# Performance work log

Hardware: AMD Instinct MI355X
Metric: run time of the kernel (lower is better)

The kernel has to match this reference:

```python
import jax, jax.numpy as jnp
from jax import lax
import numpy as np

B, T, S, Q = 256, 128, 16, 16
E, K = 128, 20
VOCAB = 50000 + K  # vocab_size + num_blocks (key slots appended)


def prelu(x, a):
    return jnp.where(x > 0, x, a * x)


def setup_inputs() -> dict:
    key = jax.random.key(0)
    ks = jax.random.split(key, 12)
    story = jax.random.randint(ks[0], (B, T, S), 0, 50000, dtype=jnp.int64 if jax.config.jax_enable_x64 else jnp.int32)
    query = jax.random.randint(ks[1], (B, Q), 0, 50000, dtype=jnp.int64 if jax.config.jax_enable_x64 else jnp.int32)
    embed_table = jax.random.normal(ks[2], (VOCAB, E), jnp.float32) * 0.1
    embed_table = embed_table.at[0].set(0.0)  # padding_idx=0
    story_mask = jnp.ones((S, E), jnp.float32)
    query_mask = jnp.ones((Q, E), jnp.float32)
    prelu_a = jnp.ones((E,), jnp.float32)
    U = jax.random.normal(ks[3], (E, E), jnp.float32) * 0.1
    V = jax.random.normal(ks[4], (E, E), jnp.float32) * 0.1
    W = jax.random.normal(ks[5], (E, E), jnp.float32) * 0.1
    bias = jax.random.normal(ks[6], (E,), jnp.float32) * 0.1
    H = jax.random.normal(ks[7], (E, E), jnp.float32) * 0.1
    R = jax.random.normal(ks[8], (VOCAB, E), jnp.float32) * 0.1
    return {"story": story, "query": query, "embed_table": embed_table,
            "story_mask": story_mask, "query_mask": query_mask, "prelu_a": prelu_a,
            "U": U, "V": V, "W": W, "bias": bias, "H": H, "R": R}


def reference(story, query, embed_table, story_mask, query_mask, prelu_a, U, V, W, bias, H, R):
    # encode story: (B,T,S,E) * (S,E) summed over S -> (B,T,E)
    s_enc = jnp.sum(embed_table[story] * story_mask, axis=2)
    # encode query: (B,Q,E) * (Q,E) summed over Q -> (B,E)
    q_enc = jnp.sum(embed_table[query] * query_mask, axis=1)

    keys = embed_table[VOCAB - K:]              # (K,E) block keys
    state0 = jnp.broadcast_to(keys[None], (B, K, E))
    key_V = keys @ V.T                           # (K,E), loop-invariant

    def step(state, x):                          # state (B,K,E), x (B,E)
        gate = jax.nn.sigmoid(jnp.einsum('be,bke->bk', x, state) + x @ keys.T)  # (B,K)
        cand = prelu(jnp.einsum('bke,fe->bkf', state, U) + bias
                     + (x @ W.T)[:, None, :] + key_V[None], prelu_a)
        ns = state + gate[..., None] * cand
        norm = jnp.linalg.norm(ns, axis=-1, keepdims=True) + 1e-8
        ns = jnp.where(ns > 0, ns, 1.0) / norm   # Threshold(0,1) then L2-normalize
        return ns, None

    state, _ = lax.scan(step, state0, jnp.swapaxes(s_enc, 0, 1))  # scan over T

    # output module
    att = jax.nn.softmax(jnp.einsum('bke,be->bk', state, q_enc), axis=-1)
    u = jnp.einsum('bk,bke->be', att, state)
    y = prelu(q_enc + u @ H.T, prelu_a) @ R.T    # (B,VOCAB)
    return y
```

## Files before the change

### kernel.cpp

```cpp
#include <hip/hip_runtime.h>
#include <hip/hip_bf16.h>
#include <stdint.h>

#define BB 256
#define TT 128
#define SS 16
#define QQ 16
#define EE 128
#define KK 20
#define VOCAB 50020
#define KB_ROWS 10
#define XK_STR 24

typedef __attribute__((ext_vector_type(8))) _Float16 h8v;
typedef __attribute__((ext_vector_type(2))) __fp16 fp2v;
typedef __attribute__((ext_vector_type(4))) unsigned short u4h;
typedef __attribute__((ext_vector_type(4))) float f4v;
#define MFMA16(a,b,c) __builtin_amdgcn_mfma_f32_16x16x32_f16(a,b,c,0,0,0)

static __device__ __forceinline__ unsigned pk2u(fp2v h){
  union { fp2v h; unsigned u; } c; c.h = h; return c.u;
}
static __device__ __forceinline__ float pk_lo(fp2v h){ return (float)h[0]; }
static __device__ __forceinline__ float pk_hi(fp2v h){ return (float)h[1]; }
static __device__ __forceinline__ unsigned short h1u(_Float16 h){
  union { _Float16 h; unsigned short u; } c; c.h = h; return c.u;
}
static __device__ __forceinline__ void split2_8(const float* v, h8v& h, h8v& l){
  #pragma unroll
  for (int j=0;j<8;++j){
    _Float16 hb = (_Float16)v[j];
    float hf = (float)hb;
    h[j] = hb;
    l[j] = (_Float16)(v[j]-hf);
  }
}
static __device__ __forceinline__ float dpp_add16(float x){
  int v;
  v = __builtin_amdgcn_update_dpp(0, __float_as_int(x), 0xB1, 0xF, 0xF, true);
  x += __int_as_float(v);
  v = __builtin_amdgcn_update_dpp(0, __float_as_int(x), 0x4E, 0xF, 0xF, true);
  x += __int_as_float(v);
  v = __builtin_amdgcn_update_dpp(0, __float_as_int(x), 0x124, 0xF, 0xF, true);
  x += __int_as_float(v);
  v = __builtin_amdgcn_update_dpp(0, __float_as_int(x), 0x128, 0xF, 0xF, true);
  x += __int_as_float(v);
  return x;
}
template<int IMM>
static __device__ __forceinline__ u4h tr_read(unsigned va){
  u4h d;
  asm volatile("ds_read_b64_tr_b16 %0, %1 offset:%c2" : "=v"(d) : "v"(va), "i"(IMM));
  return d;
}
static __device__ __forceinline__ h8v cat8h(u4h a, u4h b){
  union { u4h p[2]; h8v v; } u; u.p[0]=a; u.p[1]=b; return u.v;
}
#define LDA(P,K4) cat8h(tr_read<(P)*4096+(K4)*1024>(va), tr_read<(P)*4096+(K4)*1024+128>(va))

static const size_t OFF_SENC = 0;
static const size_t OFF_QENC = OFF_SENC + (size_t)BB*TT*EE;
static const size_t OFF_CKF  = OFF_QENC + (size_t)BB*EE;
static const size_t OFF_XW   = OFF_CKF  + (size_t)KK*EE;
static const size_t OFF_Z    = OFF_XW   + (size_t)BB*TT*EE;
static const size_t OFF_XK   = OFF_Z    + (size_t)BB*EE;
static const size_t OFF_ST   = OFF_XK   + (size_t)BB*TT*XK_STR;

__global__ __launch_bounds__(256) void k_small(
    const int* __restrict__ query, const float* __restrict__ emb,
    const float* __restrict__ qmask, const float* __restrict__ V,
    const float* __restrict__ bias, float* __restrict__ qenc,
    float* __restrict__ Ckf)
{
  int tid = threadIdx.x;
  int bid = blockIdx.x;
  if (bid < BB/8){
    int row = bid*8 + (tid>>5);
    int e4 = (tid&31)*4;
    float4 acc = make_float4(0.f,0.f,0.f,0.f);
    #pragma unroll
    for (int s=0; s<QQ; ++s) {
      int id = query[row*QQ + s];
      float4 ev = *(const float4*)(emb + (size_t)id*EE + e4);
      float4 mv = *(const float4*)(qmask + s*EE + e4);
      acc.x += ev.x*mv.x; acc.y += ev.y*mv.y; acc.z += ev.z*mv.z; acc.w += ev.w*mv.w;
    }
    *(float4*)(qenc + (size_t)row*EE + e4) = acc;
  } else {
    int k = bid - BB/8;
    if (tid < 128){
      int f = tid;
      const float* key = emb + (size_t)(VOCAB-KK+k)*EE;
      const float* vr  = V + (size_t)f*EE;
      float acc = bias[f];
      for (int e=0; e<EE; e+=4) {
        float4 kv = *(const float4*)(key + e);
        float4 vv = *(const float4*)(vr + e);
        acc += kv.x*vv.x + kv.y*vv.y + kv.z*vv.z + kv.w*vv.w;
      }
      Ckf[k*EE + f] = acc;
    }
  }
}

__global__ __launch_bounds__(256) void k_enc_xw(
    const int* __restrict__ tok, const float* __restrict__ emb,
    const float* __restrict__ smask, const float* __restrict__ W,
    float* __restrict__ senc, float* __restrict__ xw,
    float* __restrict__ xk)
{
  __shared__ float xs[64*EE];
  __shared__ float keys_s[KK*EE];
  int tid = threadIdx.x;
  int r0 = blockIdx.x*64;
  for (int i=0;i<8;++i){
    int row = i*8 + (tid>>5);
    int e4 = (tid&31)*4;
    float4 acc = make_float4(0.f,0.f,0.f,0.f);
    #pragma unroll
    for (int s=0; s<SS; ++s) {
      int id = tok[(size_t)(r0+row)*SS + s];
      float4 ev = *(const float4*)(emb + (size_t)id*EE + e4);
      float4 mv = *(const float4*)(smask + s*EE + e4);
      acc.x += ev.x*mv.x; acc.y += ev.y*mv.y; acc.z += ev.z*mv.z; acc.w += ev.w*mv.w;
    }
    *(float4*)(xs + row*EE + e4) = acc;
    *(float4*)(senc + (size_t)(r0+row)*EE + e4) = acc;
  }
  for (int idx=tid; idx<KK*EE; idx+=256)
    keys_s[idx] = emb[(size_t)(VOCAB-KK + (idx>>7))*EE + (idx&127)];
  __syncthreads();
  int f  = tid & 127;
  int rh = tid >> 7;
  float acc[32];
  #pragma unroll
  for (int i=0;i<32;++i) acc[i]=0.f;
  const float* wr = W + (size_t)f*EE;
  for (int e4=0; e4<EE; e4+=4) {
    float4 w4 = *(const float4*)(wr + e4);
    #pragma unroll
    for (int rr=0; rr<32; ++rr) {
      float4 x4 = *(const float4*)(xs + (rh*32+rr)*EE + e4);
      acc[rr] += w4.x*x4.x + w4.y*x4.y + w4.z*x4.z + w4.w*x4.w;
    }
  }
  #pragma unroll
  for (int rr=0; rr<32; ++rr)
    xw[(size_t)(r0 + rh*32 + rr)*EE + f] = acc[rr];
  for (int i=0;i<5;++i){
    int task = tid + i*256;
    int r = task/KK, k = task - r*KK;
    float a = 0.f;
    for (int e=0; e<EE; e+=4){
      float4 x4 = *(const float4*)(xs + r*EE + e);
      float4 k4 = *(const float4*)(keys_s + k*EE + e);
      a += x4.x*k4.x + x4.y*k4.y + x4.z*k4.z + x4.w*k4.w;
    }
    int ki = k < 10 ? k : k + 2;
    xk[(size_t)(r0+r)*XK_STR + ki] = a;
  }
}

struct ScanLds {
  unsigned short st[2][2][EE][16];
  unsigned short xp[2][2][EE];
  float npart[2][4][16];
};

__global__ __launch_bounds__(256) void k_scan(
    const float* __restrict__ emb, const float* __restrict__ U,
    const float* __restrict__ senc, const float* __restrict__ xw,
    const float* __restrict__ xk, const float* __restrict__ Ckf,
    const float* __restrict__ prelu_a, float* __restrict__ zst)
{
  __shared__ ScanLds L;
  int tid = threadIdx.x;
  int bid = blockIdx.x;
  int b   = bid >> 1, kb = bid & 1;
  int l   = tid & 63, cg = tid >> 6;
  int q   = l >> 4,  c  = l & 15;
  int col[2] = { cg*32 + c, cg*32 + 16 + c };

  for (int idx = tid; idx < 2*2*EE*16; idx += 256) ((unsigned short*)L.st)[idx] = 0;
  __syncthreads();
  for (int idx = tid; idx < KB_ROWS*EE; idx += 256){
    int row = idx >> 7, e = idx & 127;
    float v = emb[(size_t)(VOCAB - KK + kb*KB_ROWS + row)*EE + e];
    _Float16 hb = (_Float16)v;
    _Float16 lb = (_Float16)(v - (float)hb);
    L.st[0][0][e][row] = h1u(hb);
    L.st[0][1][e][row] = h1u(lb);
  }
  h8v bh[2][4], bl[2][4];
  #pragma unroll
  for (int nt=0;nt<2;++nt)
    #pragma unroll
    for (int kk=0;kk<4;++kk){
      float tmp[8];
      const float* up = U + (size_t)col[nt]*EE + kk*32 + q*8;
      *(float4*)&tmp[0] = *(const float4*)up;
      *(float4*)&tmp[4] = *(const float4*)(up+4);
      split2_8(tmp, bh[nt][kk], bl[nt][kk]);
    }
  float Creg[2][4], pa2[2], nsv[2][4];
  bool realr[4];
  #pragma unroll
  for (int r=0;r<4;++r) realr[r] = (4*q + r) < KB_ROWS;
  #pragma unroll
  for (int nt=0;nt<2;++nt){
    pa2[nt] = prelu_a[col[nt]];
    #pragma unroll
    for (int r=0;r<4;++r){
      int lr = 4*q + r;
      Creg[nt][r] = realr[r] ? Ckf[(kb*KB_ROWS+lr)*EE + col[nt]] : 0.f;
      nsv[nt][r]  = realr[r] ? emb[(size_t)(VOCAB-KK+kb*KB_ROWS+lr)*EE + col[nt]] : 0.f;
    }
  }

  const float* xrow  = senc + (size_t)b*TT*EE;
  const float* xwrow = xw   + (size_t)b*TT*EE;
  const float* xkrow = xk   + (size_t)b*TT*XK_STR + kb*12;

  if (tid < EE){
    float v = xrow[tid];
    _Float16 hb = (_Float16)v;
    _Float16 lb = (_Float16)(v - (float)hb);
    L.xp[0][0][tid] = h1u(hb); L.xp[0][1][tid] = h1u(lb);
  }
  float xwc[2] = { xwrow[col[0]], xwrow[col[1]] };
  float xkc[4];
  {
    f4v xk4 = {0.f,0.f,0.f,0.f};
    if (q < 3) xk4 = *(const f4v*)(xkrow + 4*q);
    #pragma unroll
    for (int r=0;r<4;++r) xkc[r] = realr[r] ? xk4[r] : 0.f;
  }

  unsigned va0 = (unsigned)(uintptr_t)&L.st[0][0][0][0] + q*256 + c*8;
  __syncthreads();

  for (int t=0; t<TT; ++t){
    int p = t & 1, pn = p ^ 1;
    unsigned va = va0 + p*8192;
    const unsigned short (*xpp)[EE] = L.xp[p];

    float invr[4];
    if (t > 0){
      f4v p0 = *(const f4v*)&L.npart[p][0][4*q];
      f4v p1 = *(const f4v*)&L.npart[p][1][4*q];
      f4v p2 = *(const f4v*)&L.npart[p][2][4*q];
      f4v p3 = *(const f4v*)&L.npart[p][3][4*q];
      f4v ss = p0 + p1 + p2 + p3;
      #pragma unroll
      for (int r=0;r<4;++r)
        invr[r] = __builtin_amdgcn_rcpf(__builtin_amdgcn_sqrtf(ss[r]) + 1e-8f);
    } else {
      #pragma unroll
      for (int r=0;r<4;++r) invr[r] = 1.0f;
    }

    float nxv = 0.f, xwn[2] = {0.f,0.f};
    f4v xk4n = {0.f,0.f,0.f,0.f};
    if (t+1 < TT){
      if (tid < EE) nxv = xrow[(size_t)(t+1)*EE + tid];
      xwn[0] = xwrow[(size_t)(t+1)*EE + col[0]];
      xwn[1] = xwrow[(size_t)(t+1)*EE + col[1]];
      if (q < 3) xk4n = *(const f4v*)(xkrow + (size_t)(t+1)*XK_STR + 4*q);
    }

    h8v Ah[4] = { LDA(0,0), LDA(0,1), LDA(0,2), LDA(0,3) };
    h8v Al[4] = { LDA(1,0), LDA(1,1), LDA(1,2), LDA(1,3) };
    asm volatile("s_waitcnt lgkmcnt(0)" ::: "memory");
    __builtin_amdgcn_sched_barrier(0);

    f4v z4 = {0.f,0.f,0.f,0.f};
    f4v acc[2][2] = {{z4,z4},{z4,z4}};
    f4v gac[2] = {z4,z4};
    #pragma unroll
    for (int kk=0; kk<4; ++kk){
      int h = kk>>1;
      h8v xh = *(const h8v*)&xpp[0][kk*32 + q*8];
      h8v xl = *(const h8v*)&xpp[1][kk*32 + q*8];
      #pragma unroll
      for (int nt=0;nt<2;++nt){
        acc[nt][h] = MFMA16(Al[kk], bh[nt][kk], acc[nt][h]);
        acc[nt][h] = MFMA16(Ah[kk], bl[nt][kk], acc[nt][h]);
        acc[nt][h] = MFMA16(Ah[kk], bh[nt][kk], acc[nt][h]);
      }
      gac[h] = MFMA16(Al[kk], xh, gac[h]);
      gac[h] = MFMA16(Ah[kk], xl, gac[h]);
      gac[h] = MFMA16(Ah[kk], xh, gac[h]);
    }
    f4v acc0 = acc[0][0] + acc[0][1];
    f4v acc1 = acc[1][0] + acc[1][1];
    f4v gacc = gac[0] + gac[1];

    float s2[4];
    #pragma unroll
    for (int r=0;r<4;++r){
      float graw = gacc[r]*invr[r] + xkc[r];
      float g = __builtin_amdgcn_rcpf(1.0f + __builtin_amdgcn_exp2f(-1.442695040889f * graw));
      float s2r = 0.f;
      #pragma unroll
      for (int nt=0;nt<2;++nt){
        float so = nsv[nt][r] * invr[r];
        float cv = (nt ? acc1[r] : acc0[r])*invr[r] + Creg[nt][r] + xwc[nt];
        cv = cv > 0.f ? cv : pa2[nt]*cv;
        float n = so + g*cv;
        nsv[nt][r] = realr[r] ? (n > 0.f ? n : 1.0f) : 0.f;
        s2r += n*n;
      }
      s2[r] = dpp_add16(s2r);
    }
    if (c == 0){
      f4v np; np[0]=s2[0]; np[1]=s2[1]; np[2]=s2[2]; np[3]=s2[3];
      *(f4v*)&L.npart[pn][cg][4*q] = np;
    }

    #pragma unroll
    for (int nt=0;nt<2;++nt){
      float v0=nsv[nt][0], v1=nsv[nt][1], v2=nsv[nt][2], v3=nsv[nt][3];
      fp2v pa = __builtin_amdgcn_cvt_pkrtz(v0, v1);
      fp2v pb = __builtin_amdgcn_cvt_pkrtz(v2, v3);
      float r0 = v0 - pk_lo(pa);
      float r1 = v1 - pk_hi(pa);
      float r2 = v2 - pk_lo(pb);
      float r3 = v3 - pk_hi(pb);
      fp2v pc = __builtin_amdgcn_cvt_pkrtz(r0, r1);
      fp2v pd = __builtin_amdgcn_cvt_pkrtz(r2, r3);
      *(uint2*)&L.st[pn][0][col[nt]][4*q] = make_uint2(pk2u(pa), pk2u(pb));
      *(uint2*)&L.st[pn][1][col[nt]][4*q] = make_uint2(pk2u(pc), pk2u(pd));
    }
    if (t+1 < TT && tid < EE){
      _Float16 hb = (_Float16)nxv;
      _Float16 lb = (_Float16)(nxv - (float)hb);
      L.xp[pn][0][tid] = h1u(hb); L.xp[pn][1][tid] = h1u(lb);
    }
    xwc[0]=xwn[0]; xwc[1]=xwn[1];
    #pragma unroll
    for (int r=0;r<4;++r) xkc[r] = realr[r] ? xk4n[r] : 0.f;
    __syncthreads();
  }

  {
    int pf = TT & 1;
    f4v p0 = *(const f4v*)&L.npart[pf][0][4*q];
    f4v p1 = *(const f4v*)&L.npart[pf][1][4*q];
    f4v p2 = *(const f4v*)&L.npart[pf][2][4*q];
    f4v p3 = *(const f4v*)&L.npart[pf][3][4*q];
    f4v ss = p0 + p1 + p2 + p3;
    #pragma unroll
    for (int r=0;r<4;++r){
      if (realr[r]){
        float inv = __builtin_amdgcn_rcpf(__builtin_amdgcn_sqrtf(ss[r]) + 1e-8f);
        #pragma unroll
        for (int nt=0;nt<2;++nt)
          zst[((size_t)b*KK + kb*KB_ROWS + 4*q + r)*EE + col[nt]] = nsv[nt][r]*inv;
      }
    }
  }
}

__global__ __launch_bounds__(128) void k_tail(
    const float* __restrict__ zst, const float* __restrict__ qenc,
    const float* __restrict__ prelu_a, const float* __restrict__ H,
    float* __restrict__ zout)
{
  __shared__ float st[KK*EE];
  __shared__ float us[EE];
  __shared__ float red[2][KK];
  __shared__ float gs[KK];
  int b = blockIdx.x, tid = threadIdx.x;
  for (int i = tid; i < KK*EE; i += 128) st[i] = zst[(size_t)b*KK*EE + i];
  float qv = qenc[(size_t)b*EE + tid];
  __syncthreads();
  int wv = tid >> 6, ln = tid & 63;
  for (int k=0;k<KK;++k){
    float p = qv * st[k*EE + tid];
    #pragma unroll
    for (int off=32; off; off>>=1) p += __shfl_xor(p, off);
    if (ln == 0) red[wv][k] = p;
  }
  __syncthreads();
  if (tid == 0){
    float mx = -1e30f, gg[KK];
    for (int k=0;k<KK;++k){ float v = red[0][k]+red[1][k]; gg[k]=v; mx = fmaxf(mx, v); }
    float s = 0.f;
    for (int k=0;k<KK;++k){ float e_ = expf(gg[k]-mx); gg[k]=e_; s += e_; }
    for (int k=0;k<KK;++k) gs[k] = gg[k]/s;
  }
  __syncthreads();
  float u_ = 0.f;
  #pragma unroll
  for (int k=0;k<KK;++k) u_ += gs[k]*st[k*EE + tid];
  us[tid] = u_;
  __syncthreads();
  float hp = 0.f;
  const float* hr = H + (size_t)tid*EE;
  for (int e=0; e<EE; e+=4){
    float4 h4 = *(const float4*)(hr + e);
    float4 u4 = *(const float4*)(us + e);
    hp += h4.x*u4.x + h4.y*u4.y + h4.z*u4.z + h4.w*u4.w;
  }
  float zv = qv + hp;
  float pat = prelu_a[tid];
  zv = zv > 0.f ? zv : pat*zv;
  zout[(size_t)b*EE + tid] = zv;
}

__global__ __launch_bounds__(256) void k_out(
    const float* __restrict__ z, const float* __restrict__ R,
    float* __restrict__ y)
{
  int tid = threadIdx.x;
  int w = tid >> 6, l = tid & 63;
  int q = l >> 4, cc = l & 15;
  int b0 = blockIdx.y * 64;
  int vbase = blockIdx.x * 256 + w * 64;

  h8v ah[4][4], al[4][4];
  #pragma unroll
  for (int mt=0;mt<4;++mt){
    const float* zr = z + (size_t)(b0 + mt*16 + cc)*EE;
    #pragma unroll
    for (int kk=0;kk<4;++kk){
      float tmp[8];
      *(float4*)&tmp[0] = *(const float4*)(zr + kk*32 + q*8);
      *(float4*)&tmp[4] = *(const float4*)(zr + kk*32 + q*8 + 4);
      split2_8(tmp, ah[mt][kk], al[mt][kk]);
    }
  }
  #pragma unroll
  for (int vt=0; vt<4; ++vt){
    int v = vbase + vt*16 + cc;
    int vc = v < VOCAB ? v : VOCAB-1;
    const float* rr = R + (size_t)vc*EE;
    h8v bh[4], bl[4];
    #pragma unroll
    for (int kk=0;kk<4;++kk){
      float tmp[8];
      *(float4*)&tmp[0] = *(const float4*)(rr + kk*32 + q*8);
      *(float4*)&tmp[4] = *(const float4*)(rr + kk*32 + q*8 + 4);
      split2_8(tmp, bh[kk], bl[kk]);
    }
    f4v acc0 = {0.f,0.f,0.f,0.f};
    f4v acc1 = {0.f,0.f,0.f,0.f};
    f4v acc2 = {0.f,0.f,0.f,0.f};
    f4v acc3 = {0.f,0.f,0.f,0.f};
    #pragma unroll
    for (int kk=0;kk<4;++kk){
      acc0 = MFMA16(al[0][kk], bh[kk], acc0);
      acc0 = MFMA16(ah[0][kk], bl[kk], acc0);
      acc0 = MFMA16(ah[0][kk], bh[kk], acc0);
      acc1 = MFMA16(al[1][kk], bh[kk], acc1);
      acc1 = MFMA16(ah[1][kk], bl[kk], acc1);
      acc1 = MFMA16(ah[1][kk], bh[kk], acc1);
      acc2 = MFMA16(al[2][kk], bh[kk], acc2);
      acc2 = MFMA16(ah[2][kk], bl[kk], acc2);
      acc2 = MFMA16(ah[2][kk], bh[kk], acc2);
      acc3 = MFMA16(al[3][kk], bh[kk], acc3);
      acc3 = MFMA16(ah[3][kk], bl[kk], acc3);
      acc3 = MFMA16(ah[3][kk], bh[kk], acc3);
    }
    if (v < VOCAB){
      #pragma unroll
      for (int r=0;r<4;++r){
        y[(size_t)(b0 +      q*4 + r)*VOCAB + v] = acc0[r];
        y[(size_t)(b0 + 16 + q*4 + r)*VOCAB + v] = acc1[r];
        y[(size_t)(b0 + 32 + q*4 + r)*VOCAB + v] = acc2[r];
        y[(size_t)(b0 + 48 + q*4 + r)*VOCAB + v] = acc3[r];
      }
    }
  }
}

extern "C" void kernel_launch(void* const* d_in, const int* in_sizes, int n_in,
                              void* d_out, int out_size, void* d_ws, size_t ws_size,
                              hipStream_t stream)
{
  const int*   story = (const int*)d_in[0];
  const int*   query = (const int*)d_in[1];
  const float* emb   = (const float*)d_in[2];
  const float* smask = (const float*)d_in[3];
  const float* qmask = (const float*)d_in[4];
  const float* pa    = (const float*)d_in[5];
  const float* U     = (const float*)d_in[6];
  const float* V     = (const float*)d_in[7];
  const float* W     = (const float*)d_in[8];
  const float* bias  = (const float*)d_in[9];
  const float* H     = (const float*)d_in[10];
  const float* R     = (const float*)d_in[11];
  float* y  = (float*)d_out;
  float* ws = (float*)d_ws;

  float* s_enc = ws + OFF_SENC;
  float* q_enc = ws + OFF_QENC;
  float* Ckf   = ws + OFF_CKF;
  float* xw    = ws + OFF_XW;
  float* z     = ws + OFF_Z;
  float* xk    = ws + OFF_XK;
  float* zst   = ws + OFF_ST;

  k_small<<<dim3(BB/8 + KK), 256, 0, stream>>>(query, emb, qmask, V, bias, q_enc, Ckf);
  k_enc_xw<<<dim3(BB*TT/64), 256, 0, stream>>>(story, emb, smask, W, s_enc, xw, xk);

  k_scan<<<dim3(BB*2), 256, 0, stream>>>(emb, U, s_enc, xw, xk, Ckf, pa, zst);
  k_tail<<<dim3(BB), 128, 0, stream>>>(zst, q_enc, pa, H, z);

  k_out<<<dim3((VOCAB+255)/256, BB/64), 256, 0, stream>>>(z, R, y);
}
```

Measured before the change: 390.8 us.

## Precompute fp16 copy of R and drop its low-part MFMA correction

A merged prologue kernel now converts R to fp16 once per call, and computes the story and query encodings plus the key/V term. The old encode+xW kernel becomes a pure xW kernel that reads s_enc from global memory. In the output GEMM only the z operand stays split into high and low fp16 parts, so the ah*bl MFMA term is removed and R is read as half-width data. This cuts MFMA work and R bandwidth in k_out, at the cost of an extra pass over R for conversion and lower precision for R (fp16 rounding of its values).

```diff
diff --git a/kernel.cpp b/kernel.cpp
--- a/kernel.cpp
+++ b/kernel.cpp
@@ -11,6 +11,10 @@
 #define VOCAB 50020
 #define KB_ROWS 10
 #define XK_STR 24
+
+#define NCVT  3127
+#define NSTORY (BB*TT/8)
+#define NQUERY (BB/8)
 
 typedef __attribute__((ext_vector_type(8))) _Float16 h8v;
 typedef __attribute__((ext_vector_type(2))) __fp16 fp2v;
@@ -65,29 +69,54 @@
 static const size_t OFF_Z    = OFF_XW   + (size_t)BB*TT*EE;
 static const size_t OFF_XK   = OFF_Z    + (size_t)BB*EE;
 static const size_t OFF_ST   = OFF_XK   + (size_t)BB*TT*XK_STR;
-
-__global__ __launch_bounds__(256) void k_small(
-    const int* __restrict__ query, const float* __restrict__ emb,
+static const size_t OFF_RH   = OFF_ST   + (size_t)BB*KK*EE;
+
+__global__ __launch_bounds__(256) void k_pro(
+    const int* __restrict__ story, const int* __restrict__ query,
+    const float* __restrict__ emb, const float* __restrict__ smask,
     const float* __restrict__ qmask, const float* __restrict__ V,
-    const float* __restrict__ bias, float* __restrict__ qenc,
-    float* __restrict__ Ckf)
+    const float* __restrict__ bias, const float* __restrict__ R,
+    float* __restrict__ senc, float* __restrict__ qenc,
+    float* __restrict__ Ckf, unsigned short* __restrict__ Rh)
 {
+  int bid = blockIdx.x;
   int tid = threadIdx.x;
-  int bid = blockIdx.x;
-  if (bid < BB/8){
-    int row = bid*8 + (tid>>5);
+  if (bid < NCVT){
+    size_t i = ((size_t)bid*256 + tid)*8;
+    if (i >= (size_t)VOCAB*EE) return;
+    float tmp[8];
+    *(float4*)&tmp[0] = *(const float4*)(R+i);
+    *(float4*)&tmp[4] = *(const float4*)(R+i+4);
+    h8v h;
+    #pragma unroll
+    for (int j=0;j<8;++j) h[j] = (_Float16)tmp[j];
+    *(h8v*)(Rh+i) = h;
+  } else if (bid < NCVT + NSTORY){
+    int row = (bid - NCVT)*8 + (tid>>5);
     int e4 = (tid&31)*4;
     float4 acc = make_float4(0.f,0.f,0.f,0.f);
     #pragma unroll
+    for (int s=0; s<SS; ++s) {
+      int id = story[(size_t)row*SS + s];
+      float4 ev = *(const float4*)(emb + (size_t)id*EE + e4);
+      float4 mv = *(const float4*)(smask + s*EE + e4);
+      acc.x += ev.x*mv.x; acc.y += ev.y*mv.y; acc.z += ev.z*mv.z; acc.w += ev.w*mv.w;
+    }
+    *(float4*)(senc + (size_t)row*EE + e4) = acc;
+  } else if (bid < NCVT + NSTORY + NQUERY){
+    int row = (bid - NCVT - NSTORY)*8 + (tid>>5);
+    int e4 = (tid&31)*4;
+    float4 acc = make_float4(0.f,0.f,0.f,0.f);
+    #pragma unroll
     for (int s=0; s<QQ; ++s) {
-      int id = query[row*QQ + s];
+      int id = query[(size_t)row*QQ + s];
       float4 ev = *(const float4*)(emb + (size_t)id*EE + e4);
       float4 mv = *(const float4*)(qmask + s*EE + e4);
       acc.x += ev.x*mv.x; acc.y += ev.y*mv.y; acc.z += ev.z*mv.z; acc.w += ev.w*mv.w;
     }
     *(float4*)(qenc + (size_t)row*EE + e4) = acc;
   } else {
-    int k = bid - BB/8;
+    int k = bid - NCVT - NSTORY - NQUERY;
     if (tid < 128){
       int f = tid;
       const float* key = emb + (size_t)(VOCAB-KK+k)*EE;
@@ -103,10 +132,9 @@
   }
 }
 
-__global__ __launch_bounds__(256) void k_enc_xw(
-    const int* __restrict__ tok, const float* __restrict__ emb,
-    const float* __restrict__ smask, const float* __restrict__ W,
-    float* __restrict__ senc, float* __restrict__ xw,
+__global__ __launch_bounds__(256) void k_xw(
+    const float* __restrict__ senc, const float* __restrict__ W,
+    const float* __restrict__ emb, float* __restrict__ xw,
     float* __restrict__ xk)
 {
   __shared__ float xs[64*EE];
@@ -114,18 +142,8 @@
   int tid = threadIdx.x;
   int r0 = blockIdx.x*64;
   for (int i=0;i<8;++i){
-    int row = i*8 + (tid>>5);
-    int e4 = (tid&31)*4;
-    float4 acc = make_float4(0.f,0.f,0.f,0.f);
-    #pragma unroll
-    for (int s=0; s<SS; ++s) {
-      int id = tok[(size_t)(r0+row)*SS + s];
-      float4 ev = *(const float4*)(emb + (size_t)id*EE + e4);
-      float4 mv = *(const float4*)(smask + s*EE + e4);
-      acc.x += ev.x*mv.x; acc.y += ev.y*mv.y; acc.z += ev.z*mv.z; acc.w += ev.w*mv.w;
-    }
-    *(float4*)(xs + row*EE + e4) = acc;
-    *(float4*)(senc + (size_t)(r0+row)*EE + e4) = acc;
+    int idx = tid + i*256; int r = idx>>5; int c4 = (idx&31)*4;
+    *(float4*)(xs + r*EE + c4) = *(const float4*)(senc + (size_t)(r0+r)*EE + c4);
   }
   for (int idx=tid; idx<KK*EE; idx+=256)
     keys_s[idx] = emb[(size_t)(VOCAB-KK + (idx>>7))*EE + (idx&127)];
@@ -409,7 +427,7 @@
 }
 
 __global__ __launch_bounds__(256) void k_out(
-    const float* __restrict__ z, const float* __restrict__ R,
+    const float* __restrict__ z, const unsigned short* __restrict__ Rh,
     float* __restrict__ y)
 {
   int tid = threadIdx.x;
@@ -434,15 +452,11 @@
   for (int vt=0; vt<4; ++vt){
     int v = vbase + vt*16 + cc;
     int vc = v < VOCAB ? v : VOCAB-1;
-    const float* rr = R + (size_t)vc*EE;
-    h8v bh[4], bl[4];
-    #pragma unroll
-    for (int kk=0;kk<4;++kk){
-      float tmp[8];
-      *(float4*)&tmp[0] = *(const float4*)(rr + kk*32 + q*8);
-      *(float4*)&tmp[4] = *(const float4*)(rr + kk*32 + q*8 + 4);
-      split2_8(tmp, bh[kk], bl[kk]);
-    }
+    const unsigned short* rr = Rh + (size_t)vc*EE;
+    h8v bh[4];
+    #pragma unroll
+    for (int kk=0;kk<4;++kk)
+      bh[kk] = *(const h8v*)(rr + kk*32 + q*8);
     f4v acc0 = {0.f,0.f,0.f,0.f};
     f4v acc1 = {0.f,0.f,0.f,0.f};
     f4v acc2 = {0.f,0.f,0.f,0.f};
@@ -450,16 +464,12 @@
     #pragma unroll
     for (int kk=0;kk<4;++kk){
       acc0 = MFMA16(al[0][kk], bh[kk], acc0);
-      acc0 = MFMA16(ah[0][kk], bl[kk], acc0);
       acc0 = MFMA16(ah[0][kk], bh[kk], acc0);
       acc1 = MFMA16(al[1][kk], bh[kk], acc1);
-      acc1 = MFMA16(ah[1][kk], bl[kk], acc1);
       acc1 = MFMA16(ah[1][kk], bh[kk], acc1);
       acc2 = MFMA16(al[2][kk], bh[kk], acc2);
-      acc2 = MFMA16(ah[2][kk], bl[kk], acc2);
       acc2 = MFMA16(ah[2][kk], bh[kk], acc2);
       acc3 = MFMA16(al[3][kk], bh[kk], acc3);
-      acc3 = MFMA16(ah[3][kk], bl[kk], acc3);
       acc3 = MFMA16(ah[3][kk], bh[kk], acc3);
     }
     if (v < VOCAB){
@@ -500,12 +510,14 @@
   float* z     = ws + OFF_Z;
   float* xk    = ws + OFF_XK;
   float* zst   = ws + OFF_ST;
-
-  k_small<<<dim3(BB/8 + KK), 256, 0, stream>>>(query, emb, qmask, V, bias, q_enc, Ckf);
-  k_enc_xw<<<dim3(BB*TT/64), 256, 0, stream>>>(story, emb, smask, W, s_enc, xw, xk);
+  unsigned short* Rh = (unsigned short*)(ws + OFF_RH);
+
+  k_pro<<<dim3(NCVT + NSTORY + NQUERY + KK), 256, 0, stream>>>(
+      story, query, emb, smask, qmask, V, bias, R, s_enc, q_enc, Ckf, Rh);
+  k_xw<<<dim3(BB*TT/64), 256, 0, stream>>>(s_enc, W, emb, xw, xk);
 
   k_scan<<<dim3(BB*2), 256, 0, stream>>>(emb, U, s_enc, xw, xk, Ckf, pa, zst);
   k_tail<<<dim3(BB), 128, 0, stream>>>(zst, q_enc, pa, H, z);
 
-  k_out<<<dim3((VOCAB+255)/256, BB/64), 256, 0, stream>>>(z, R, y);
-}
+  k_out<<<dim3((VOCAB+255)/256, BB/64), 256, 0, stream>>>(z, Rh, y);
+}
```

After: 363.5 us (median of 2 runs). 1.08x faster.
